# Kernel optimization log

Hardware: AMD Instinct MI355X
Metric: run time of the kernel (lower is better)

Reference implementation:

```python
import jax, jax.numpy as jnp
import numpy as np

B, V, D, NH, DH = 1, 6, 256, 8, 32
L, ZP = 4, 4
BEV = 80
Q = BEV * BEV
SHAPES = [(56, 100), (28, 50), (14, 25), (7, 13)]
N = sum(h * w for h, w in SHAPES)
PAD_H, PAD_W = 448, 800
PC = (-48.0, -48.0, -5.0, 48.0, 48.0, 3.0)
EPS = 1e-5


def _ref3d():
    # get_reference_points + pc_range scaling; the original overwrites the z channel
    # with scaled-x (code bug: ref_3d[...,2:3] = ref_3d[...,:1]*zrange+zmin) -> reproduced faithfully,
    # so all ZP pillar points are identical.
    u = jnp.arange(Q)
    xs = ((u % BEV).astype(jnp.float32) + 0.5) / BEV
    ys = ((u // BEV).astype(jnp.float32) + 0.5) / BEV
    x = xs * (PC[3] - PC[0]) + PC[0]
    y = ys * (PC[4] - PC[1]) + PC[1]
    z = x * (PC[5] - PC[2]) + PC[2]
    p = jnp.stack([x, y, z], -1)  # [Q,3]
    return jnp.broadcast_to(p[None], (ZP, Q, 3))


def _project(l2i):
    # l2i: [B,V,4,4] -> normalized coords [B,V,Q,ZP,2], validity mask [B,V,Q,ZP]
    pts = _ref3d().reshape(-1, 3)
    pts_h = jnp.concatenate([pts, jnp.ones_like(pts[:, :1])], -1)  # [ZP*Q,4]
    ip = jnp.einsum('bvij,nj->bvni', l2i, pts_h)                   # [B,V,ZP*Q,4]
    zc = ip[..., 2]
    xy = ip[..., :2] / jnp.clip(zc, EPS, None)[..., None]
    xn = xy[..., 0] / PAD_W
    yn = xy[..., 1] / PAD_H
    m = (zc > EPS) & (xn > 0) & (xn < 1) & (yn > 0) & (yn < 1)
    coords = jnp.stack([xn, yn], -1).reshape(B, V, ZP, Q, 2).transpose(0, 1, 3, 2, 4)
    mask = m.reshape(B, V, ZP, Q).transpose(0, 1, 3, 2)
    return coords, mask


def _forward(feat0, feat1, feat2, feat3, lidar2img_mat, bev_emb, level_embeds,
             view_embeds, value_W, value_b, off_W, off_b, aw_W, aw_b, out_W, out_b):
    feats = [feat0, feat1, feat2, feat3]
    parts = []
    for l, f in enumerate(feats):
        h, w = SHAPES[l]
        x = f.reshape(B, V, D, h * w).transpose(0, 1, 3, 2)  # [B,V,hw,D]
        x = x + view_embeds[None, :, None, :] + level_embeds[l]
        parts.append(x)
    feat_flat = jnp.concatenate(parts, axis=2)  # [B,V,N,D]

    coords, mask = _project(lidar2img_mat)
    mask_any = mask.any(-1)                                            # [B,V,Q]
    count = jnp.clip(mask_any.sum(1).astype(jnp.float32), 1.0, None)   # [B,Q]

    value = (feat_flat.reshape(B * V, N, D) @ value_W + value_b).reshape(B * V, N, NH, DH)
    off = (bev_emb @ off_W + off_b).reshape(Q, NH, L, ZP, 2)
    aw = jax.nn.softmax((bev_emb @ aw_W + aw_b).reshape(Q, NH, L * ZP), -1).reshape(Q, NH, L, ZP)
    ref = coords.reshape(B * V, Q, ZP, 2)

    out = jnp.zeros((B * V, Q, NH, DH), feat_flat.dtype)
    start = 0
    for l, (h, w) in enumerate(SHAPES):
        v_l = value[:, start:start + h * w].transpose(0, 2, 1, 3).reshape(B * V * NH, h * w, DH)
        start += h * w
        loc = ref[:, :, None, :, :] + off[None, :, :, l] / jnp.array([w, h], feat_flat.dtype)
        loc = loc.transpose(0, 2, 1, 3, 4).reshape(B * V * NH, Q * ZP, 2)
        # grid_sample(align_corners=False, padding='zeros') with grid 2*loc-1
        gx = loc[..., 0] * w - 0.5
        gy = loc[..., 1] * h - 0.5
        x0 = jnp.floor(gx).astype(jnp.int32)
        y0 = jnp.floor(gy).astype(jnp.int32)
        wx1 = gx - x0
        wy1 = gy - y0

        def corner(xi, yi, wt):
            valid = (xi >= 0) & (xi < w) & (yi >= 0) & (yi < h)
            lin = jnp.clip(yi, 0, h - 1) * w + jnp.clip(xi, 0, w - 1)
            g = jnp.take_along_axis(v_l, lin[..., None], axis=1)
            return g * (wt * valid)[..., None]

        s = (corner(x0, y0, (1 - wx1) * (1 - wy1)) + corner(x0 + 1, y0, wx1 * (1 - wy1))
             + corner(x0, y0 + 1, (1 - wx1) * wy1) + corner(x0 + 1, y0 + 1, wx1 * wy1))
        s = s.reshape(B * V, NH, Q, ZP, DH)
        out = out + jnp.einsum('vhqzd,qhz->vqhd', s, aw[:, :, l])

    attn = out.reshape(B, V, Q, D)
    slots = (attn * mask_any[..., None]).sum(1) / count[..., None]
    slots = slots @ out_W + out_b
    return bev_emb[None] + slots  # dropout is identity at inference


def setup_inputs() -> dict:
    key = jax.random.key(0)
    ks = jax.random.split(key, 16)
    s = 0.02
    return {
        'feat0': jax.random.normal(ks[0], (B, V, D) + SHAPES[0], jnp.float32),
        'feat1': jax.random.normal(ks[1], (B, V, D) + SHAPES[1], jnp.float32),
        'feat2': jax.random.normal(ks[2], (B, V, D) + SHAPES[2], jnp.float32),
        'feat3': jax.random.normal(ks[3], (B, V, D) + SHAPES[3], jnp.float32),
        'lidar2img_mat': jax.random.normal(ks[4], (B, V, 4, 4), jnp.float32) * 50.0,
        'bev_emb': jax.random.normal(ks[5], (Q, D), jnp.float32) * s,
        'level_embeds': jax.random.normal(ks[6], (L, D), jnp.float32) * s,
        'view_embeds': jax.random.normal(ks[7], (V, D), jnp.float32) * s,
        'value_W': jax.random.normal(ks[8], (D, D), jnp.float32) * s,
        'value_b': jnp.zeros((D,), jnp.float32),
        'off_W': jax.random.normal(ks[9], (D, NH * L * ZP * 2), jnp.float32) * s,
        'off_b': jnp.zeros((NH * L * ZP * 2,), jnp.float32),
        'aw_W': jax.random.normal(ks[10], (D, NH * L * ZP), jnp.float32) * s,
        'aw_b': jnp.zeros((NH * L * ZP,), jnp.float32),
        'out_W': jax.random.normal(ks[11], (D, D), jnp.float32) * s,
        'out_b': jnp.zeros((D,), jnp.float32),
    }


def reference(feat0, feat1, feat2, feat3, lidar2img_mat, bev_emb, level_embeds,
              view_embeds, value_W, value_b, off_W, off_b, aw_W, aw_b, out_W, out_b):
    return _forward(feat0, feat1, feat2, feat3, lidar2img_mat, bev_emb, level_embeds,
                    view_embeds, value_W, value_b, off_W, off_b, aw_W, aw_b, out_W, out_b)
```

## Files before the change

### kernel.cpp

```cpp
#include <hip/hip_runtime.h>
#include <cstdint>
#include <cstddef>

#define NV 6
#define ND 256
#define NHEAD 8
#define NBEV 80
#define NQ 6400
#define NTOK 7441
#define MROWS (NV * NTOK)
#define MROWSP 44672
#define FEPS 1e-5f

#define VBLKS 698
#define GBLKS 848
#define GCHUNK (GBLKS / 8)

#define PR_PROJ 150
#define PR_TR   2832
#define PR_BEV  800
#define PB0 PR_PROJ
#define PB1 (PB0 + PR_TR)
#define PB2 (PB1 + PR_BEV)
#define PB3 (PB2 + 256)
#define PB4 (PB3 + 256)
#define PB5 (PB4 + 128)
#define PB6 (PB5 + 256)
#define PBT (PB6 + 24)

typedef __attribute__((ext_vector_type(8))) short bfx8;
typedef __attribute__((ext_vector_type(4))) float fx4;

__device__ __forceinline__ unsigned short f2bf(float x) {
    uint32_t u = __builtin_bit_cast(uint32_t, x);
    u += 0x7FFFu + ((u >> 16) & 1u);
    return (unsigned short)(u >> 16);
}
__device__ __forceinline__ float lof(uint32_t u) {
    return __builtin_bit_cast(float, u << 16);
}
__device__ __forceinline__ float hif(uint32_t u) {
    return __builtin_bit_cast(float, u & 0xFFFF0000u);
}
__device__ __forceinline__ unsigned short f2h(float x) {
    return __builtin_bit_cast(unsigned short, (_Float16)x);
}
__device__ __forceinline__ float h2f(unsigned short h) {
    return (float)__builtin_bit_cast(_Float16, h);
}

__global__ __launch_bounds__(256) void k_prep(
        const float* __restrict__ f0, const float* __restrict__ f1,
        const float* __restrict__ f2, const float* __restrict__ f3,
        const float* __restrict__ l2i, const float* __restrict__ bev,
        const float* __restrict__ ve, const float* __restrict__ le,
        const float* __restrict__ vW, const float* __restrict__ vB,
        const float* __restrict__ oW, const float* __restrict__ aW,
        const float* __restrict__ outW,
        float2* __restrict__ coords, int* __restrict__ mask,
        unsigned short* __restrict__ featT, unsigned short* __restrict__ bevh,
        unsigned short* __restrict__ vWt, unsigned short* __restrict__ oaWt,
        unsigned short* __restrict__ outWt, float* __restrict__ emb_proj) {
    int bid = blockIdx.x;
    int t = threadIdx.x;
    if (bid < PB0) {
        int idx = bid * 256 + t;
        int v = idx / NQ, q = idx - v * NQ;
        float xs = ((float)(q % NBEV) + 0.5f) / (float)NBEV;
        float ys = ((float)(q / NBEV) + 0.5f) / (float)NBEV;
        float x = xs * 96.0f - 48.0f;
        float y = ys * 96.0f - 48.0f;
        float z = x * 8.0f - 5.0f;
        const float* M = l2i + v * 16;
        float ip0 = M[0] * x + M[1] * y + M[2] * z + M[3];
        float ip1 = M[4] * x + M[5] * y + M[6] * z + M[7];
        float ip2 = M[8] * x + M[9] * y + M[10] * z + M[11];
        float dz = fmaxf(ip2, FEPS);
        float xn = ip0 / dz / 800.0f;
        float yn = ip1 / dz / 448.0f;
        bool m = (ip2 > FEPS) && (xn > 0.0f) && (xn < 1.0f) && (yn > 0.0f) && (yn < 1.0f);
        coords[idx] = make_float2(xn, yn);
        mask[idx] = m ? 1 : 0;
    } else if (bid < PB1) {
        __shared__ float T[64][65];
        int idx = bid - PB0;
        int v = idx / 472;
        int rem = idx - v * 472;
        int mt = rem >> 2, kt = rem & 3;
        int hw, p0, st;
        const float* base;
        if (mt < 88)       { base = f0; hw = 5600; st = 0;    p0 = mt * 64; }
        else if (mt < 110) { base = f1; hw = 1400; st = 5600; p0 = (mt - 88) * 64; }
        else if (mt < 116) { base = f2; hw = 350;  st = 7000; p0 = (mt - 110) * 64; }
        else               { base = f3; hw = 91;   st = 7350; p0 = (mt - 116) * 64; }
        int k0 = kt * 64;
        const float* src = base + (size_t)v * 256 * hw;
#pragma unroll
        for (int i = 0; i < 16; ++i) {
            int ii = t + i * 256;
            int kk = ii >> 6, mm = ii & 63;
            float val = (p0 + mm < hw) ? src[(size_t)(k0 + kk) * hw + p0 + mm] : 0.0f;
            T[kk][mm] = val;
        }
        __syncthreads();
        size_t row0 = (size_t)v * NTOK + st + p0;
        int slot = t & 7;
#pragma unroll
        for (int j = 0; j < 2; ++j) {
            int mm = (t >> 3) + j * 32;
            if (p0 + mm < hw) {
                bfx8 o;
#pragma unroll
                for (int jj = 0; jj < 8; ++jj)
                    o[jj] = (short)f2bf(T[slot * 8 + jj][mm]);
                *(bfx8*)&featT[(row0 + mm) * 256 + k0 + slot * 8] = o;
            }
        }
    } else if (bid < PB2) {
        size_t e = (size_t)(bid - PB1) * 2048 + t * 8;
        float4 a = *(const float4*)(bev + e);
        float4 b = *(const float4*)(bev + e + 4);
        bfx8 o;
        o[0] = (short)f2bf(a.x); o[1] = (short)f2bf(a.y);
        o[2] = (short)f2bf(a.z); o[3] = (short)f2bf(a.w);
        o[4] = (short)f2bf(b.x); o[5] = (short)f2bf(b.y);
        o[6] = (short)f2bf(b.z); o[7] = (short)f2bf(b.w);
        *(bfx8*)(bevh + e) = o;
    } else if (bid < PB3) {
        int e = (bid - PB2) * 256 + t;
        int k = e >> 8, n = e & 255;
        vWt[(size_t)n * 256 + k] = f2bf(vW[(size_t)k * 256 + n]);
    } else if (bid < PB4) {
        int e = (bid - PB3) * 256 + t;
        int k = e >> 8, n = e & 255;
        oaWt[(size_t)n * 256 + k] = f2bf(oW[(size_t)k * 256 + n]);
    } else if (bid < PB5) {
        int e = (bid - PB4) * 256 + t;
        int k = e >> 7, n = e & 127;
        oaWt[(size_t)(256 + n) * 256 + k] = f2bf(aW[(size_t)k * 128 + n]);
    } else if (bid < PB6) {
        int e = (bid - PB5) * 256 + t;
        int k = e >> 8, n = e & 255;
        outWt[(size_t)n * 256 + k] = f2bf(outW[(size_t)k * 256 + n]);
    } else {
        int blk = bid - PB6;
        int v = blk >> 2, l = blk & 3;
        float acc = vB[t];
        for (int d = 0; d < ND; ++d)
            acc += (ve[v * ND + d] + le[l * ND + d]) * vW[d * ND + t];
        emb_proj[blk * ND + t] = acc;
    }
}

__global__ __launch_bounds__(256) void k_gemms(
        const unsigned short* __restrict__ featT,
        const unsigned short* __restrict__ vWt, const float* __restrict__ emb_proj,
        unsigned short* __restrict__ value,
        const unsigned short* __restrict__ bevh,
        const unsigned short* __restrict__ oaWt,
        const float* __restrict__ oB, const float* __restrict__ aB,
        float* __restrict__ off, float* __restrict__ aw_pre) {
    __shared__ unsigned short As[128][40];
    __shared__ unsigned short Bs[128][40];
    int b = blockIdx.x;
    int lb = (b & 7) * GCHUNK + (b >> 3);
    int t = threadIdx.x;
    int lane = t & 63, w = t >> 6;
    int wm = w >> 1, wn = w & 1;
    int lr = lane & 15, lk = lane >> 4;

    bool isval = lb < VBLKS;
    int m0, c0;
    const unsigned short *ap, *bp;
    if (isval) {
        m0 = (lb >> 1) * 128; c0 = (lb & 1) * 128;
        ap = featT; bp = vWt;
    } else {
        int r6 = lb - VBLKS;
        m0 = (r6 / 3) * 128; c0 = (r6 % 3) * 128;
        ap = bevh; bp = oaWt;
    }
    int sr = t & 127, skh = (t >> 7) * 16;
    const unsigned short* arow = ap + (size_t)(m0 + sr) * 256 + skh;
    const unsigned short* brow = bp + (size_t)(c0 + sr) * 256 + skh;

    fx4 acc[4][4];
#pragma unroll
    for (int i = 0; i < 4; ++i)
#pragma unroll
        for (int j = 0; j < 4; ++j) acc[i][j] = (fx4)0.0f;

    bfx8 ar0 = *(const bfx8*)arow;
    bfx8 ar1 = *(const bfx8*)(arow + 8);
    bfx8 br0 = *(const bfx8*)brow;
    bfx8 br1 = *(const bfx8*)(brow + 8);
#pragma unroll
    for (int k0 = 0; k0 < 256; k0 += 32) {
        *(bfx8*)&As[sr][skh]     = ar0;
        *(bfx8*)&As[sr][skh + 8] = ar1;
        *(bfx8*)&Bs[sr][skh]     = br0;
        *(bfx8*)&Bs[sr][skh + 8] = br1;
        __syncthreads();
        if (k0 < 224) {
            ar0 = *(const bfx8*)(arow + k0 + 32);
            ar1 = *(const bfx8*)(arow + k0 + 40);
            br0 = *(const bfx8*)(brow + k0 + 32);
            br1 = *(const bfx8*)(brow + k0 + 40);
        }
        bfx8 bfv[4];
#pragma unroll
        for (int f = 0; f < 4; ++f)
            bfv[f] = *(bfx8*)&Bs[wn * 64 + f * 16 + lr][lk * 8];
#pragma unroll
        for (int fm = 0; fm < 4; ++fm) {
            bfx8 afv = *(bfx8*)&As[wm * 64 + fm * 16 + lr][lk * 8];
#pragma unroll
            for (int fn = 0; fn < 4; ++fn)
                acc[fm][fn] = __builtin_amdgcn_mfma_f32_16x16x32_bf16(
                    afv, bfv[fn], acc[fm][fn], 0, 0, 0);
        }
        __syncthreads();
    }

    if (isval) {
#pragma unroll
        for (int fm = 0; fm < 4; ++fm) {
#pragma unroll
            for (int r = 0; r < 4; ++r) {
                int m = m0 + wm * 64 + fm * 16 + lk * 4 + r;
                if (m >= MROWS) continue;
                int v = m / NTOK;
                int n = m - v * NTOK;
                int l = (n < 5600) ? 0 : (n < 7000) ? 1 : (n < 7350) ? 2 : 3;
                const float* ep = emb_proj + (size_t)(v * 4 + l) * ND;
#pragma unroll
                for (int fn = 0; fn < 4; ++fn) {
                    int col = c0 + wn * 64 + fn * 16 + lr;
                    value[(size_t)m * ND + col] = f2bf(acc[fm][fn][r] + ep[col]);
                }
            }
        }
    } else if (c0 < 256) {
#pragma unroll
        for (int fm = 0; fm < 4; ++fm) {
#pragma unroll
            for (int fn = 0; fn < 4; ++fn) {
                int col = c0 + wn * 64 + fn * 16 + lr;
                float bs = oB[col];
#pragma unroll
                for (int r = 0; r < 4; ++r) {
                    int m = m0 + wm * 64 + fm * 16 + lk * 4 + r;
                    off[(size_t)m * 256 + col] = acc[fm][fn][r] + bs;
                }
            }
        }
    } else {
#pragma unroll
        for (int fm = 0; fm < 4; ++fm) {
#pragma unroll
            for (int fn = 0; fn < 4; ++fn) {
                int col = wn * 64 + fn * 16 + lr;
                float bs = aB[col];
#pragma unroll
                for (int r = 0; r < 4; ++r) {
                    int m = m0 + wm * 64 + fm * 16 + lk * 4 + r;
                    aw_pre[(size_t)m * 128 + col] = acc[fm][fn][r] + bs;
                }
            }
        }
    }
}

#define SQB 2
__global__ __launch_bounds__(256) void k_sample(
        const float2* __restrict__ coords, const int* __restrict__ mask,
        const float* __restrict__ off, const float* __restrict__ awlog,
        const unsigned short* __restrict__ value, float* __restrict__ slots) {
    __shared__ float aw_s[SQB][128];
    __shared__ uint4 lw_s[SQB][NV][128];
    __shared__ float2 cxy_s[SQB][NV];
    __shared__ int msk_s[SQB][NV];

    int b = blockIdx.x;
    int lb = (b & 7) * (NQ / SQB / 8) + (b >> 3);
    int q0 = lb * SQB;
    int t = threadIdx.x;
    if (t < SQB * NV) {
        int qq = t / NV, v = t - qq * NV;
        msk_s[qq][v] = mask[v * NQ + q0 + qq];
        cxy_s[qq][v] = coords[v * NQ + q0 + qq];
    }
    {
        int qq = t >> 7, c2 = t & 127;
        aw_s[qq][c2] = awlog[(size_t)(q0 + qq) * 128 + c2];
    }
    __syncthreads();
    if (t < SQB * NHEAD) {
        int qq = t >> 3, h = t & 7;
        float* p = &aw_s[qq][h * 16];
        float mx = p[0];
#pragma unroll
        for (int i = 1; i < 16; ++i) mx = fmaxf(mx, p[i]);
        float e[16];
        float s = 0.0f;
#pragma unroll
        for (int i = 0; i < 16; ++i) { e[i] = __expf(p[i] - mx); s += e[i]; }
        float inv = 1.0f / s;
#pragma unroll
        for (int i = 0; i < 16; ++i) p[i] = e[i] * inv;
    }
    __syncthreads();

    const int LW[4] = {100, 50, 25, 13};
    const int LH[4] = {56, 28, 14, 7};
    const int LST[4] = {0, 5600, 7000, 7350};
    for (int idx = t; idx < SQB * NV * 128; idx += 256) {
        int c2 = idx & 127;
        int rem = idx >> 7;
        int qq = rem / NV, v = rem - qq * NV;
        if (!msk_s[qq][v]) continue;
        int ll = (c2 >> 2) & 3;
        int iwl = LW[ll], ihl = LH[ll], st = LST[ll];
        float wl = (float)iwl, hl = (float)ihl;
        float2 o2 = *(const float2*)&off[(size_t)(q0 + qq) * 256 + 2 * c2];
        float2 cc = cxy_s[qq][v];
        float gx = cc.x * wl + o2.x - 0.5f;
        float gy = cc.y * hl + o2.y - 0.5f;
        float fxf = floorf(gx), fyf = floorf(gy);
        int x0 = (int)fxf, y0 = (int)fyf;
        float wx = gx - fxf, wy = gy - fyf;
        bool bx0 = (unsigned)x0 < (unsigned)iwl;
        bool bx1 = (unsigned)(x0 + 1) < (unsigned)iwl;
        bool by0 = (unsigned)y0 < (unsigned)ihl;
        bool by1 = (unsigned)(y0 + 1) < (unsigned)ihl;
        int cx0 = min(max(x0, 0), iwl - 1);
        int cx1 = min(max(x0 + 1, 0), iwl - 1);
        int cy0 = min(max(y0, 0), ihl - 1);
        int cy1 = min(max(y0 + 1, 0), ihl - 1);
        float wa = aw_s[qq][c2];
        int r0 = st + cy0 * iwl, r1 = st + cy1 * iwl;
        float w00 = (bx0 && by0) ? (1.0f - wx) * (1.0f - wy) * wa : 0.0f;
        float w01 = (bx1 && by0) ? wx * (1.0f - wy) * wa : 0.0f;
        float w10 = (bx0 && by1) ? (1.0f - wx) * wy * wa : 0.0f;
        float w11 = (bx1 && by1) ? wx * wy * wa : 0.0f;
        uint4 lw;
        lw.x = (uint32_t)(unsigned short)(r0 + cx0) | ((uint32_t)(unsigned short)(r0 + cx1) << 16);
        lw.y = (uint32_t)(unsigned short)(r1 + cx0) | ((uint32_t)(unsigned short)(r1 + cx1) << 16);
        lw.z = (uint32_t)f2h(w00) | ((uint32_t)f2h(w01) << 16);
        lw.w = (uint32_t)f2h(w10) | ((uint32_t)f2h(w11) << 16);
        lw_s[qq][v][c2] = lw;
    }
    __syncthreads();

    int qq = t >> 7, cp = t & 127;
    int hb = (cp >> 4) * 16;
    float acc0 = 0.0f, acc1 = 0.0f;
    int cnt = 0;
#pragma unroll
    for (int v = 0; v < NV; ++v) cnt += msk_s[qq][v];
    for (int v = 0; v < NV; ++v) {
        if (!msk_s[qq][v]) continue;
        const uint32_t* vb = (const uint32_t*)(value + (size_t)v * NTOK * 256) + cp;
#pragma unroll
        for (int ci = 0; ci < 16; ++ci) {
            uint4 lw = lw_s[qq][v][hb + ci];
            uint32_t u0 = vb[(size_t)(lw.x & 0xFFFF) * 128];
            uint32_t u1 = vb[(size_t)(lw.x >> 16) * 128];
            uint32_t u2 = vb[(size_t)(lw.y & 0xFFFF) * 128];
            uint32_t u3 = vb[(size_t)(lw.y >> 16) * 128];
            float w0 = h2f((unsigned short)(lw.z & 0xFFFF));
            float w1 = h2f((unsigned short)(lw.z >> 16));
            float w2 = h2f((unsigned short)(lw.w & 0xFFFF));
            float w3 = h2f((unsigned short)(lw.w >> 16));
            acc0 += w0 * lof(u0) + w1 * lof(u1) + w2 * lof(u2) + w3 * lof(u3);
            acc1 += w0 * hif(u0) + w1 * hif(u1) + w2 * hif(u2) + w3 * hif(u3);
        }
    }
    float invc = 1.0f / fmaxf((float)cnt, 1.0f);
    *(float2*)&slots[(size_t)(q0 + qq) * 256 + 2 * cp] = make_float2(acc0 * invc, acc1 * invc);
}

__global__ __launch_bounds__(256) void k_out(
        const float* __restrict__ A, const unsigned short* __restrict__ Bt,
        const float* __restrict__ bias, const float* __restrict__ addsrc,
        float* __restrict__ out) {
    __shared__ unsigned short As[64][40];
    __shared__ unsigned short Bs[128][40];
    int t = threadIdx.x;
    int m0 = blockIdx.x * 64, c0 = blockIdx.y * 128;
    int lane = t & 63, w = t >> 6;
    int wm = w >> 1, wn = w & 1;
    int lr = lane & 15, lk = lane >> 4;
    int mA = t & 63, kg = t >> 6;
    const float* ap = A + (size_t)(m0 + mA) * 256 + kg * 8;
    const unsigned short* bp = Bt + (size_t)(c0 + (t >> 1)) * 256 + (t & 1) * 16;
    fx4 acc[2][4];
#pragma unroll
    for (int i = 0; i < 2; ++i)
#pragma unroll
        for (int j = 0; j < 4; ++j) acc[i][j] = (fx4)0.0f;

    float4 va0 = *(const float4*)ap;
    float4 va1 = *(const float4*)(ap + 4);
    bfx8 brg = *(const bfx8*)bp;
    bfx8 brg2 = *(const bfx8*)(bp + 8);
#pragma unroll
    for (int k0 = 0; k0 < 256; k0 += 32) {
        bfx8 a8;
        a8[0] = (short)f2bf(va0.x); a8[1] = (short)f2bf(va0.y);
        a8[2] = (short)f2bf(va0.z); a8[3] = (short)f2bf(va0.w);
        a8[4] = (short)f2bf(va1.x); a8[5] = (short)f2bf(va1.y);
        a8[6] = (short)f2bf(va1.z); a8[7] = (short)f2bf(va1.w);
        *(bfx8*)&As[mA][kg * 8] = a8;
        *(bfx8*)&Bs[t >> 1][(t & 1) * 16] = brg;
        *(bfx8*)&Bs[t >> 1][(t & 1) * 16 + 8] = brg2;
        __syncthreads();
        if (k0 < 224) {
            va0 = *(const float4*)(ap + k0 + 32);
            va1 = *(const float4*)(ap + k0 + 36);
            brg = *(const bfx8*)(bp + k0 + 32);
            brg2 = *(const bfx8*)(bp + k0 + 40);
        }
        bfx8 bfv[4];
#pragma unroll
        for (int f = 0; f < 4; ++f)
            bfv[f] = *(bfx8*)&Bs[wn * 64 + f * 16 + lr][lk * 8];
#pragma unroll
        for (int fm = 0; fm < 2; ++fm) {
            bfx8 afv = *(bfx8*)&As[wm * 32 + fm * 16 + lr][lk * 8];
#pragma unroll
            for (int fn = 0; fn < 4; ++fn)
                acc[fm][fn] = __builtin_amdgcn_mfma_f32_16x16x32_bf16(
                    afv, bfv[fn], acc[fm][fn], 0, 0, 0);
        }
        __syncthreads();
    }
#pragma unroll
    for (int fm = 0; fm < 2; ++fm) {
#pragma unroll
        for (int fn = 0; fn < 4; ++fn) {
            int col = c0 + wn * 64 + fn * 16 + lr;
            float bs = bias[col];
#pragma unroll
            for (int r = 0; r < 4; ++r) {
                int m = m0 + wm * 32 + fm * 16 + lk * 4 + r;
                out[(size_t)m * 256 + col] =
                    acc[fm][fn][r] + bs + addsrc[(size_t)m * 256 + col];
            }
        }
    }
}

extern "C" void kernel_launch(void* const* d_in, const int* in_sizes, int n_in,
                              void* d_out, int out_size, void* d_ws, size_t ws_size,
                              hipStream_t stream) {
    const float* f0   = (const float*)d_in[0];
    const float* f1   = (const float*)d_in[1];
    const float* f2   = (const float*)d_in[2];
    const float* f3   = (const float*)d_in[3];
    const float* l2i  = (const float*)d_in[4];
    const float* bev  = (const float*)d_in[5];
    const float* le   = (const float*)d_in[6];
    const float* ve   = (const float*)d_in[7];
    const float* vW   = (const float*)d_in[8];
    const float* vB   = (const float*)d_in[9];
    const float* oW   = (const float*)d_in[10];
    const float* oB   = (const float*)d_in[11];
    const float* aW   = (const float*)d_in[12];
    const float* aB   = (const float*)d_in[13];
    const float* outW = (const float*)d_in[14];
    const float* outB = (const float*)d_in[15];
    float* out = (float*)d_out;

    char* ws = (char*)d_ws;
    size_t o = 0;
    auto alloc = [&](size_t bytes) {
        void* p = ws + o;
        o += (bytes + 255) & ~(size_t)255;
        return p;
    };
    float2* coords   = (float2*)alloc((size_t)NV * NQ * sizeof(float2));
    int*    mask     = (int*)alloc((size_t)NV * NQ * sizeof(int));
    float*  emb_proj = (float*)alloc((size_t)24 * ND * sizeof(float));
    float*  off      = (float*)alloc((size_t)NQ * 256 * sizeof(float));
    float*  aw_pre   = (float*)alloc((size_t)NQ * 128 * sizeof(float));
    float*  slots    = (float*)alloc((size_t)NQ * 256 * sizeof(float));
    unsigned short* value = (unsigned short*)alloc((size_t)MROWS * ND * sizeof(short));
    unsigned short* featT = (unsigned short*)alloc((size_t)MROWSP * ND * sizeof(short));
    unsigned short* bevh  = (unsigned short*)alloc((size_t)NQ * ND * sizeof(short));
    unsigned short* vWt   = (unsigned short*)alloc((size_t)256 * 256 * sizeof(short));
    unsigned short* oaWt  = (unsigned short*)alloc((size_t)384 * 256 * sizeof(short));
    unsigned short* outWt = (unsigned short*)alloc((size_t)256 * 256 * sizeof(short));

    k_prep<<<PBT, 256, 0, stream>>>(f0, f1, f2, f3, l2i, bev, ve, le, vW, vB,
                                    oW, aW, outW, coords, mask, featT, bevh,
                                    vWt, oaWt, outWt, emb_proj);
    k_gemms<<<GBLKS, 256, 0, stream>>>(featT, vWt, emb_proj, value,
                                       bevh, oaWt, oB, aB, off, aw_pre);
    k_sample<<<NQ / SQB, 256, 0, stream>>>(coords, mask, off, aw_pre, value, slots);
    dim3 gout(NQ / 64, 2);
    k_out<<<gout, 256, 0, stream>>>(slots, outWt, outB, bev, out);
}
```

Baseline: 190.4 us.

## Double-buffer GEMM tiles via direct global-to-LDS loads with XOR swizzle

Reworks the k_gemms main loop. Tiles now move straight from global memory into LDS with global_load_lds 16-byte transfers, skipping the round trip through registers. K steps are 64 wide instead of 32, and the loop runs double-buffered with one barrier per step, so the next chunk loads while the current one feeds the MFMAs. An XOR swizzle of the 16-byte slots replaces the padded LDS rows to avoid bank conflicts. It uses more LDS per block (64 KB), which may lower occupancy. It also depends on correct wait counts for the asynchronous LDS writes before each barrier.

```diff
diff --git a/kernel.cpp b/kernel.cpp
--- a/kernel.cpp
+++ b/kernel.cpp
@@ -30,6 +30,13 @@
 
 typedef __attribute__((ext_vector_type(8))) short bfx8;
 typedef __attribute__((ext_vector_type(4))) float fx4;
+
+typedef __attribute__((address_space(3))) unsigned int lds_u32_t;
+typedef __attribute__((address_space(1))) const unsigned int glb_u32_t;
+
+__device__ __forceinline__ void gload16(const unsigned short* g, unsigned short* l) {
+    __builtin_amdgcn_global_load_lds((glb_u32_t*)g, (lds_u32_t*)l, 16, 0, 0);
+}
 
 __device__ __forceinline__ unsigned short f2bf(float x) {
     uint32_t u = __builtin_bit_cast(uint32_t, x);
@@ -160,8 +167,7 @@
         const unsigned short* __restrict__ oaWt,
         const float* __restrict__ oB, const float* __restrict__ aB,
         float* __restrict__ off, float* __restrict__ aw_pre) {
-    __shared__ unsigned short As[128][40];
-    __shared__ unsigned short Bs[128][40];
+    __shared__ unsigned short LDS[4 * 8192];
     int b = blockIdx.x;
     int lb = (b & 7) * GCHUNK + (b >> 3);
     int t = threadIdx.x;
@@ -180,9 +186,11 @@
         m0 = (r6 / 3) * 128; c0 = (r6 % 3) * 128;
         ap = bevh; bp = oaWt;
     }
-    int sr = t & 127, skh = (t >> 7) * 16;
-    const unsigned short* arow = ap + (size_t)(m0 + sr) * 256 + skh;
-    const unsigned short* brow = bp + (size_t)(c0 + sr) * 256 + skh;
+
+    int rsub = lane >> 3;
+    int kslx = (lane & 7) ^ rsub;
+    const unsigned short* asrc = ap + (size_t)(m0 + w * 32 + rsub) * 256 + kslx * 8;
+    const unsigned short* bsrc = bp + (size_t)(c0 + w * 32 + rsub) * 256 + kslx * 8;
 
     fx4 acc[4][4];
 #pragma unroll
@@ -190,36 +198,44 @@
 #pragma unroll
         for (int j = 0; j < 4; ++j) acc[i][j] = (fx4)0.0f;
 
-    bfx8 ar0 = *(const bfx8*)arow;
-    bfx8 ar1 = *(const bfx8*)(arow + 8);
-    bfx8 br0 = *(const bfx8*)brow;
-    bfx8 br1 = *(const bfx8*)(brow + 8);
-#pragma unroll
-    for (int k0 = 0; k0 < 256; k0 += 32) {
-        *(bfx8*)&As[sr][skh]     = ar0;
-        *(bfx8*)&As[sr][skh + 8] = ar1;
-        *(bfx8*)&Bs[sr][skh]     = br0;
-        *(bfx8*)&Bs[sr][skh + 8] = br1;
+    auto STAGE = [&](int c, int buf) {
+        const unsigned short* a = asrc + c * 64;
+        const unsigned short* bb = bsrc + c * 64;
+        unsigned short* la = &LDS[(buf * 2 + 0) * 8192 + w * 2048];
+        unsigned short* lbp = &LDS[(buf * 2 + 1) * 8192 + w * 2048];
+#pragma unroll
+        for (int j = 0; j < 4; ++j) {
+            gload16(a + j * 2048, la + j * 512);
+            gload16(bb + j * 2048, lbp + j * 512);
+        }
+    };
+    auto COMPUTE = [&](int buf) {
+        const char* Ab = (const char*)&LDS[(buf * 2 + 0) * 8192] + (wm * 64 + lr) * 128;
+        const char* Bb = (const char*)&LDS[(buf * 2 + 1) * 8192] + (wn * 64 + lr) * 128;
+#pragma unroll
+        for (int s = 0; s < 2; ++s) {
+            int xs = (((s * 4 + lk) ^ (lr & 7)) << 4);
+            bfx8 bfv[4];
+#pragma unroll
+            for (int f = 0; f < 4; ++f)
+                bfv[f] = *(const bfx8*)(Bb + f * 2048 + xs);
+#pragma unroll
+            for (int fm = 0; fm < 4; ++fm) {
+                bfx8 afv = *(const bfx8*)(Ab + fm * 2048 + xs);
+#pragma unroll
+                for (int fn = 0; fn < 4; ++fn)
+                    acc[fm][fn] = __builtin_amdgcn_mfma_f32_16x16x32_bf16(
+                        afv, bfv[fn], acc[fm][fn], 0, 0, 0);
+            }
+        }
+    };
+
+    STAGE(0, 0);
+#pragma unroll
+    for (int c = 0; c < 4; ++c) {
         __syncthreads();
-        if (k0 < 224) {
-            ar0 = *(const bfx8*)(arow + k0 + 32);
-            ar1 = *(const bfx8*)(arow + k0 + 40);
-            br0 = *(const bfx8*)(brow + k0 + 32);
-            br1 = *(const bfx8*)(brow + k0 + 40);
-        }
-        bfx8 bfv[4];
-#pragma unroll
-        for (int f = 0; f < 4; ++f)
-            bfv[f] = *(bfx8*)&Bs[wn * 64 + f * 16 + lr][lk * 8];
-#pragma unroll
-        for (int fm = 0; fm < 4; ++fm) {
-            bfx8 afv = *(bfx8*)&As[wm * 64 + fm * 16 + lr][lk * 8];
-#pragma unroll
-            for (int fn = 0; fn < 4; ++fn)
-                acc[fm][fn] = __builtin_amdgcn_mfma_f32_16x16x32_bf16(
-                    afv, bfv[fn], acc[fm][fn], 0, 0, 0);
-        }
-        __syncthreads();
+        if (c < 3) STAGE(c + 1, (c + 1) & 1);
+        COMPUTE(c & 1);
     }
 
     if (isval) {
```

Result: faster. 181.2 us (-4.8%).
